# Performance work log

Measured on AMD Instinct MI355X. Metric: run time of the kernel, lower is better.

## Reference

```python
import jax, jax.numpy as jnp
import numpy as np

B, S, HID = 2, 2048, 2048
NUM_HEADS, NUM_KV = 32, 8
HEAD_DIM = HID // NUM_HEADS  # 64
GROUP = NUM_HEADS // NUM_KV  # 4
SCALE = 1.0 / np.sqrt(HEAD_DIM)


def rotate_half(x):
    x1, x2 = jnp.split(x, 2, axis=-1)
    return jnp.concatenate((-x2, x1), axis=-1)


def rope_tables(seq_len, dim):
    # NOTE: original repo buggily built the table over hidden_dim; the only
    # broadcast-consistent (and standard) interpretation is per-head dim.
    inv_freq = 1.0 / (10000.0 ** (jnp.arange(0, dim, 2, dtype=jnp.float32) / dim))
    t = jnp.arange(seq_len, dtype=jnp.float32)
    freqs = t[:, None] * inv_freq[None, :]          # (S, dim/2)
    emb = jnp.concatenate((freqs, freqs), axis=-1)  # (S, dim)
    return jnp.sin(emb), jnp.cos(emb)


def setup_inputs() -> dict:
    key = jax.random.key(0)
    ks = jax.random.split(key, 6)
    hidden_states = jax.random.normal(ks[0], (B, S, HID), dtype=jnp.float32)
    # causal additive mask (intent of the module's broken else-branch)
    causal = jnp.triu(jnp.full((S, S), -1e9, dtype=jnp.float32), k=1)
    attn_mask = causal[None, None]  # (1,1,S,S)
    init = lambda k, shp: jax.random.normal(k, shp, dtype=jnp.float32) * (1.0 / np.sqrt(shp[1]))
    wq = init(ks[1], (HID, HID))
    wk = init(ks[2], (NUM_KV * HEAD_DIM, HID))
    wv = init(ks[3], (NUM_KV * HEAD_DIM, HID))
    wo = init(ks[4], (HID, HID))
    return {"hidden_states": hidden_states, "attn_mask": attn_mask,
            "wq": wq, "wk": wk, "wv": wv, "wo": wo}


def reference(hidden_states, attn_mask, wq, wk, wv, wo):
    b, s, _ = hidden_states.shape
    q = (hidden_states @ wq.T).reshape(b, s, NUM_HEADS, HEAD_DIM)
    k = (hidden_states @ wk.T).reshape(b, s, NUM_KV, HEAD_DIM)
    v = (hidden_states @ wv.T).reshape(b, s, NUM_KV, HEAD_DIM)

    sin, cos = rope_tables(s, HEAD_DIM)        # (S, D)
    sin = sin[None, :, None, :]                # (1,S,1,D)
    cos = cos[None, :, None, :]
    q = q * cos + rotate_half(q) * sin
    k = k * cos + rotate_half(k) * sin

    # GQA without materializing repeat_interleave: split query heads as (kv, group)
    q = q.transpose(0, 2, 1, 3).reshape(b, NUM_KV, GROUP, s, HEAD_DIM)  # (B,K,G,S,D)
    k = k.transpose(0, 2, 1, 3)                                          # (B,K,S,D)
    v = v.transpose(0, 2, 1, 3)                                          # (B,K,S,D)

    scores = jnp.einsum('bkgqd,bksd->bkgqs', q, k) * SCALE  # (B,K,G,Sq,Sk)
    scores = scores + attn_mask[:, :, None]                 # broadcast (1,1,1,S,S)
    attn = jax.nn.softmax(scores, axis=-1)
    out = jnp.einsum('bkgqs,bksd->bkgqd', attn, v)          # (B,K,G,S,D)
    out = out.reshape(b, NUM_HEADS, s, HEAD_DIM).transpose(0, 2, 1, 3).reshape(b, s, HID)
    return out @ wo.T
```

## Files before the change

kernel.cpp:

```cpp
#include <hip/hip_runtime.h>
#include <hip/hip_bf16.h>

#define HIDDEN 2048
#define SEQ    2048
#define BATCH  2
#define NH     32
#define NKV    8
#define GRP    4
#define HD     64
#define KVDIM  512
#define NQKV   3072
#define SC2    0.18033688011112042f
#define NBANDS 32

typedef __attribute__((ext_vector_type(8))) short short8;
typedef __attribute__((ext_vector_type(4))) short short4v;
typedef __attribute__((ext_vector_type(4))) float f32x4;
typedef __attribute__((ext_vector_type(2))) float f32x2;
typedef __attribute__((ext_vector_type(4))) unsigned short us4;
typedef __attribute__((ext_vector_type(4))) float f4;

__device__ inline float bf2f(unsigned short u) {
    union { unsigned int i; float f; } x; x.i = ((unsigned int)u) << 16; return x.f;
}
__device__ inline unsigned short f2bf(float f) {
    union { float f; unsigned int i; } x; x.f = f;
    unsigned int r = x.i + 0x7fffu + ((x.i >> 16) & 1u);
    return (unsigned short)(r >> 16);
}

__device__ __forceinline__ f32x4 mfma16(short4v a, short4v b, f32x4 c) {
#if __has_builtin(__builtin_amdgcn_mfma_f32_16x16x16bf16_1k)
    return __builtin_amdgcn_mfma_f32_16x16x16bf16_1k(a, b, c, 0, 0, 0);
#elif __has_builtin(__builtin_amdgcn_mfma_f32_16x16x16_bf16)
    return __builtin_amdgcn_mfma_f32_16x16x16_bf16(a, b, c, 0, 0, 0);
#else
    asm volatile("v_mfma_f32_16x16x16_bf16 %0, %1, %2, %0" : "+v"(c) : "v"(a), "v"(b));
    return c;
#endif
}

__device__ __forceinline__ short4v pack4bf(float a, float b, float c, float d) {
    __hip_bfloat162 lo = __float22bfloat162_rn(make_float2(a, b));
    __hip_bfloat162 hi = __float22bfloat162_rn(make_float2(c, d));
    union { __hip_bfloat162 h2[2]; short4v s; } u;
    u.h2[0] = lo; u.h2[1] = hi;
    return u.s;
}

__global__ void detect_kernel(const unsigned short* __restrict__ hs, int* __restrict__ flag)
{
    int t = threadIdx.x;
    unsigned int e = hs[2 * t] & 0x7F80u;
    bool sane = (e >= 0x3800u) && (e <= 0x4100u);
    unsigned long long m = __ballot(sane);
    if (t == 0) *flag = (__popcll(m) >= 32) ? 0 : 1;
}

__global__ __launch_bounds__(256) void cvt_all(const void* __restrict__ a, const void* __restrict__ b,
                                               const void* __restrict__ c, const void* __restrict__ d,
                                               const void* __restrict__ e,
                                               unsigned short* __restrict__ dst,
                                               const int* __restrict__ flag)
{
    const int c0 = 2097152;
    const int c1 = c0 + 1048576;
    const int c2 = c1 + 262144;
    const int c3 = c2 + 262144;
    const int c4 = c3 + 1048576;
    int i = blockIdx.x * 256 + threadIdx.x;
    if (i >= c4) return;
    const void* src; int off;
    if (i < c0)      { src = a; off = i; }
    else if (i < c1) { src = b; off = i - c0; }
    else if (i < c2) { src = c; off = i - c1; }
    else if (i < c3) { src = d; off = i - c2; }
    else             { src = e; off = i - c3; }
    if (*flag) {
        f4 v = ((const f4*)src)[off];
        us4 o = { f2bf(v[0]), f2bf(v[1]), f2bf(v[2]), f2bf(v[3]) };
        ((us4*)dst)[i] = o;
    } else {
        ((us4*)dst)[i] = ((const us4*)src)[off];
    }
}

__global__ void rope_tbl_kernel(float* __restrict__ tbl)
{
    int i = blockIdx.x * blockDim.x + threadIdx.x;
    int s = i >> 5, d = i & 31;
    float f = (float)s * __expf(-(float)d * 0.28782313662425572f);
    float sn, c;
    sincosf(f, &sn, &c);
    tbl[i * 2]     = c;
    tbl[i * 2 + 1] = sn;
}

__global__ __launch_bounds__(256) void gemm128(const unsigned short* __restrict__ X,
                                               const unsigned short* __restrict__ W,
                                               void* __restrict__ Y0,
                                               unsigned short* __restrict__ Yk,
                                               unsigned short* __restrict__ Yv,
                                               const float* __restrict__ tbl,
                                               int N, int K,
                                               const int* __restrict__ flag, int mode)
{
    __shared__ unsigned short As[2][128 * 32];
    __shared__ unsigned short Bs[2][128 * 32];

    int tid  = threadIdx.x;
    int wave = tid >> 6;
    int lane = tid & 63;
    int l15  = lane & 15;
    int quad = lane >> 4;
    int wr   = wave >> 1;
    int wc   = wave & 1;
    int m0 = blockIdx.y * 128;
    int n0 = blockIdx.x * 128;

    const unsigned short* ga = X + (size_t)(m0 + (tid >> 2)) * K + (tid & 3) * 8;
    const unsigned short* gb = W + (size_t)(n0 + (tid >> 2)) * K + (tid & 3) * 8;
    const size_t rowskip = (size_t)64 * K;

#define GLDS(gp, lp) __builtin_amdgcn_global_load_lds( \
    (__attribute__((address_space(1))) void*)(gp), \
    (__attribute__((address_space(3))) void*)(lp), 16, 0, 0)

#define STAGEG(bi, k0v) do { \
    GLDS(ga + (k0v),           &As[bi][wave * 512]); \
    GLDS(ga + rowskip + (k0v), &As[bi][2048 + wave * 512]); \
    GLDS(gb + (k0v),           &Bs[bi][wave * 512]); \
    GLDS(gb + rowskip + (k0v), &Bs[bi][2048 + wave * 512]); \
} while (0)

    f32x4 acc[4][4];
#pragma unroll
    for (int i = 0; i < 4; ++i)
#pragma unroll
        for (int j = 0; j < 4; ++j) acc[i][j] = (f32x4){0.f, 0.f, 0.f, 0.f};

    STAGEG(0, 0);
    int nk = K >> 5;
    for (int it = 0; it < nk; ++it) {
        int bi = it & 1;
        __syncthreads();
        if (it + 1 < nk) STAGEG(bi ^ 1, (it + 1) * 32);

        short8 af[4], bfr[4];
#pragma unroll
        for (int mt = 0; mt < 4; ++mt)
            af[mt] = *(const short8*)&As[bi][(wr * 64 + mt * 16 + l15) * 32 + quad * 8];
#pragma unroll
        for (int nt = 0; nt < 4; ++nt)
            bfr[nt] = *(const short8*)&Bs[bi][(wc * 64 + nt * 16 + l15) * 32 + quad * 8];
#pragma unroll
        for (int mt = 0; mt < 4; ++mt)
#pragma unroll
            for (int nt = 0; nt < 4; ++nt)
                acc[mt][nt] = __builtin_amdgcn_mfma_f32_16x16x32_bf16(af[mt], bfr[nt], acc[mt][nt], 0, 0, 0);
    }
#undef STAGEG
#undef GLDS

    if (mode == 0) {
        int out_f32 = *flag;
#pragma unroll
        for (int mt = 0; mt < 4; ++mt)
#pragma unroll
            for (int nt = 0; nt < 4; ++nt)
#pragma unroll
                for (int r = 0; r < 4; ++r) {
                    size_t idx = (size_t)(m0 + wr * 64 + mt * 16 + quad * 4 + r) * N
                               + n0 + wc * 64 + nt * 16 + l15;
                    if (out_f32) ((float*)Y0)[idx] = acc[mt][nt][r];
                    else         ((unsigned short*)Y0)[idx] = f2bf(acc[mt][nt][r]);
                }
        return;
    }

    int nbase = n0 + wc * 64;
    if (nbase < HIDDEN) {
#pragma unroll
        for (int mt = 0; mt < 4; ++mt)
#pragma unroll
            for (int nt = 0; nt < 4; ++nt)
#pragma unroll
                for (int r = 0; r < 4; ++r) acc[mt][nt][r] *= SC2;
    }
    if (nbase < HIDDEN + KVDIM) {
#pragma unroll
        for (int mt = 0; mt < 4; ++mt)
#pragma unroll
            for (int r = 0; r < 4; ++r) {
                int s = (m0 + wr * 64 + mt * 16 + quad * 4 + r) & (SEQ - 1);
                f32x2 t0 = *(const f32x2*)&tbl[(s * 32 + l15) * 2];
                f32x2 t1 = *(const f32x2*)&tbl[(s * 32 + 16 + l15) * 2];
#pragma unroll
                for (int nt = 0; nt < 2; ++nt) {
                    float c  = nt ? t1[0] : t0[0];
                    float sn = nt ? t1[1] : t0[1];
                    float x1 = acc[mt][nt][r], x2 = acc[mt][nt + 2][r];
                    acc[mt][nt][r]     = x1 * c - x2 * sn;
                    acc[mt][nt + 2][r] = x2 * c + x1 * sn;
                }
            }
    }
    if (nbase < HIDDEN) {
        unsigned short* dst = (unsigned short*)Y0;
#pragma unroll
        for (int mt = 0; mt < 4; ++mt)
#pragma unroll
            for (int nt = 0; nt < 4; ++nt)
#pragma unroll
                for (int r = 0; r < 4; ++r)
                    dst[(size_t)(m0 + wr * 64 + mt * 16 + quad * 4 + r) * HIDDEN
                        + nbase + nt * 16 + l15] = f2bf(acc[mt][nt][r]);
    } else if (nbase < HIDDEN + KVDIM) {
        int cbase = nbase - HIDDEN;
#pragma unroll
        for (int mt = 0; mt < 4; ++mt)
#pragma unroll
            for (int nt = 0; nt < 4; ++nt)
#pragma unroll
                for (int r = 0; r < 4; ++r)
                    Yk[(size_t)(m0 + wr * 64 + mt * 16 + quad * 4 + r) * KVDIM
                       + cbase + nt * 16 + l15] = f2bf(acc[mt][nt][r]);
    } else {
        int kvh = (nbase - HIDDEN - KVDIM) >> 6;
#pragma unroll
        for (int mt = 0; mt < 4; ++mt) {
            int m = m0 + wr * 64 + mt * 16 + quad * 4;
            int bb = m >> 11, s = m & (SEQ - 1);
#pragma unroll
            for (int nt = 0; nt < 4; ++nt) {
                us4 pk = { f2bf(acc[mt][nt][0]), f2bf(acc[mt][nt][1]),
                           f2bf(acc[mt][nt][2]), f2bf(acc[mt][nt][3]) };
                *(us4*)&Yv[((size_t)(bb * NKV + kvh) * HD + nt * 16 + l15) * SEQ + s] = pk;
            }
        }
    }
}

__global__ __launch_bounds__(256, 4) void flash_attn(const unsigned short* __restrict__ q,
                                                     const unsigned short* __restrict__ k,
                                                     const unsigned short* __restrict__ vt,
                                                     unsigned short* __restrict__ o)
{
    __shared__ unsigned short Kd[2][64 * 64];
    __shared__ unsigned short Vd[2][64 * 64];

    int tid  = threadIdx.x;
    int lane = tid & 63;
    int wave = tid >> 6;
    int l15  = lane & 15;
    int quad = lane >> 4;
    int h7   = l15 & 7;
    int p  = blockIdx.x;
    int hp = blockIdx.y;
    int b  = blockIdx.z;
    int kv = hp >> 1;

    int srow = wave * 8 + (lane >> 3);
    int scol = ((lane & 7) ^ (lane >> 3)) * 8;
    const unsigned short* kgl = k + (size_t)(b * SEQ + srow) * KVDIM + kv * HD + scol;
    const unsigned short* vgl = vt + ((size_t)(b * NKV + kv) * HD + srow) * SEQ + scol;

#define GLDS(gp, lp) __builtin_amdgcn_global_load_lds( \
    (__attribute__((address_space(1))) void*)(gp), \
    (__attribute__((address_space(3))) void*)(lp), 16, 0, 0)

#define STAGE(bufi, j0v) do { \
    GLDS(kgl + (size_t)(j0v) * KVDIM,        &Kd[bufi][wave * 512]); \
    GLDS(kgl + (size_t)((j0v) + 32) * KVDIM, &Kd[bufi][2048 + wave * 512]); \
    GLDS(vgl + (j0v),                        &Vd[bufi][wave * 512]); \
    GLDS(vgl + (size_t)32 * SEQ + (j0v),     &Vd[bufi][2048 + wave * 512]); \
} while (0)

    for (int ph = 0; ph < 2; ++ph) {
        int band = ph ? (NBANDS - 1 - p) : p;
        int i0 = band * 64;
        int r0 = i0 + wave * 16;

        const unsigned short* qbase = q + (size_t)(b * SEQ + r0 + l15) * HIDDEN + hp * (2 * HD) + quad * 8;
        short8 aq00 = *(const short8*)(qbase);
        short8 aq01 = *(const short8*)(qbase + 32);
        short8 aq10 = *(const short8*)(qbase + 64);
        short8 aq11 = *(const short8*)(qbase + 96);

        float la00 = 0.f, la01 = 0.f, la02 = 0.f, la03 = 0.f;
        float la10 = 0.f, la11 = 0.f, la12 = 0.f, la13 = 0.f;
        f32x4 oacc0[4], oacc1[4];
#pragma unroll
        for (int t = 0; t < 4; ++t) {
            oacc0[t] = (f32x4){0.f, 0.f, 0.f, 0.f};
            oacc1[t] = (f32x4){0.f, 0.f, 0.f, 0.f};
        }

        int ig = r0 + l15;
        int ntiles = band + 1;
        STAGE(0, 0);

        for (int jt = 0; jt < ntiles; ++jt) {
            int buf = jt & 1;
            __syncthreads();
            if (jt + 1 < ntiles) STAGE(buf ^ 1, (jt + 1) * 64);
            int j0 = jt * 64;
            bool diag = (jt == band);
            const unsigned short* Kb = &Kd[buf][0];
            const unsigned short* Vb = &Vd[buf][0];

#pragma unroll
            for (int hf = 0; hf < 2; ++hf) {
                f32x4 s0[2], s1[2];
#pragma unroll
                for (int tt = 0; tt < 2; ++tt) {
                    int row = (hf * 2 + tt) * 16 + l15;
                    short8 ka0 = *(const short8*)&Kb[row * 64 + ((quad ^ h7) * 8)];
                    short8 ka1 = *(const short8*)&Kb[row * 64 + (((4 + quad) ^ h7) * 8)];
                    f32x4 z = {0.f, 0.f, 0.f, 0.f};
                    z = __builtin_amdgcn_mfma_f32_16x16x32_bf16(ka0, aq00, z, 0, 0, 0);
                    z = __builtin_amdgcn_mfma_f32_16x16x32_bf16(ka1, aq01, z, 0, 0, 0);
                    s0[tt] = z;
                    f32x4 w = {0.f, 0.f, 0.f, 0.f};
                    w = __builtin_amdgcn_mfma_f32_16x16x32_bf16(ka0, aq10, w, 0, 0, 0);
                    w = __builtin_amdgcn_mfma_f32_16x16x32_bf16(ka1, aq11, w, 0, 0, 0);
                    s1[tt] = w;
                }
                short4v ap0[2], ap1[2];
#pragma unroll
                for (int tt = 0; tt < 2; ++tt) {
                    float p0[4], p1[4];
#pragma unroll
                    for (int r = 0; r < 4; ++r) {
                        float e0 = exp2f(s0[tt][r]);
                        float e1 = exp2f(s1[tt][r]);
                        if (diag) {
                            int j = j0 + (hf * 2 + tt) * 16 + quad * 4 + r;
                            bool ok = (j <= ig);
                            e0 = ok ? e0 : 0.f;
                            e1 = ok ? e1 : 0.f;
                        }
                        p0[r] = e0; p1[r] = e1;
                    }
                    la00 += p0[0]; la01 += p0[1]; la02 += p0[2]; la03 += p0[3];
                    la10 += p1[0]; la11 += p1[1]; la12 += p1[2]; la13 += p1[3];
                    ap0[tt] = pack4bf(p0[0], p0[1], p0[2], p0[3]);
                    ap1[tt] = pack4bf(p1[0], p1[1], p1[2], p1[3]);
                }
#pragma unroll
                for (int dt = 0; dt < 4; ++dt) {
                    int vrow = dt * 16 + l15;
                    f32x4 z0 = oacc0[dt], z1 = oacc1[dt];
#pragma unroll
                    for (int tt = 0; tt < 2; ++tt) {
                        int kb = hf * 2 + tt;
                        int vcb = (kb * 32 + quad * 8) ^ (h7 << 4);
                        short4v vv = *(const short4v*)&Vb[vrow * 64 + (vcb >> 1)];
                        z0 = mfma16(vv, ap0[tt], z0);
                        z1 = mfma16(vv, ap1[tt], z1);
                    }
                    oacc0[dt] = z0; oacc1[dt] = z1;
                }
            }
        }

        float lr0 = (la00 + la01) + (la02 + la03);
        lr0 += __shfl_xor(lr0, 16, 64);
        lr0 += __shfl_xor(lr0, 32, 64);
        float lr1 = (la10 + la11) + (la12 + la13);
        lr1 += __shfl_xor(lr1, 16, 64);
        lr1 += __shfl_xor(lr1, 32, 64);
        float inv0 = 1.0f / lr0;
        float inv1 = 1.0f / lr1;
        unsigned short* obase = o + (size_t)(b * SEQ + r0 + l15) * HIDDEN + hp * (2 * HD) + quad * 4;
#pragma unroll
        for (int dt = 0; dt < 4; ++dt) {
            us4 pk0 = { f2bf(oacc0[dt][0] * inv0), f2bf(oacc0[dt][1] * inv0),
                        f2bf(oacc0[dt][2] * inv0), f2bf(oacc0[dt][3] * inv0) };
            *(us4*)(obase + dt * 16) = pk0;
            us4 pk1 = { f2bf(oacc1[dt][0] * inv1), f2bf(oacc1[dt][1] * inv1),
                        f2bf(oacc1[dt][2] * inv1), f2bf(oacc1[dt][3] * inv1) };
            *(us4*)(obase + HD + dt * 16) = pk1;
        }

        __syncthreads();
    }
#undef STAGE
#undef GLDS
}

extern "C" void kernel_launch(void* const* d_in, const int* in_sizes, int n_in,
                              void* d_out, int out_size, void* d_ws, size_t ws_size,
                              hipStream_t stream)
{
    const void* hs = d_in[0];
    const void* wq = d_in[2];
    const void* wk = d_in[3];
    const void* wv = d_in[4];
    const void* wo = d_in[5];

    const int M = BATCH * SEQ;
    int* flag = (int*)d_ws;
    unsigned short* base = (unsigned short*)((char*)d_ws + 256);
    unsigned short* hsb  = base;
    unsigned short* wqkv = hsb + (size_t)M * HIDDEN;
    unsigned short* wob  = wqkv + (size_t)NQKV * HIDDEN;
    unsigned short* qbuf = wob + (size_t)HIDDEN * HIDDEN;
    unsigned short* kbuf = qbuf + (size_t)M * HIDDEN;
    unsigned short* vbuf = kbuf + (size_t)M * KVDIM;
    unsigned short* abuf = vbuf + (size_t)M * KVDIM;
    float* tbl = (float*)(abuf + (size_t)M * HIDDEN);

    dim3 blk(256);
    detect_kernel<<<1, 64, 0, stream>>>((const unsigned short*)hs, flag);
    rope_tbl_kernel<<<256, blk, 0, stream>>>(tbl);

    const int total4 = 2097152 + 1048576 + 262144 + 262144 + 1048576;
    cvt_all<<<(total4 + 255) / 256, blk, 0, stream>>>(hs, wq, wk, wv, wo, hsb, flag);

    gemm128<<<dim3(NQKV / 128, M / 128), blk, 0, stream>>>(hsb, wqkv, qbuf, kbuf, vbuf,
                                                           tbl, NQKV, HIDDEN, flag, 1);

    flash_attn<<<dim3(NBANDS / 2, NH / 2, BATCH), blk, 0, stream>>>(qbuf, kbuf, vbuf, abuf);

    gemm128<<<dim3(HIDDEN / 128, M / 128), blk, 0, stream>>>(abuf, wob, d_out, nullptr, nullptr,
                                                             tbl, HIDDEN, HIDDEN, flag, 0);
}
```

Before: 344.3 us.

## Triple-buffer GEMM LDS stages to keep two global loads in flight

Moves the bf16 GEMM's shared-memory staging from double to triple buffering and prefetches two k-tiles ahead. A partial `s_waitcnt vmcnt(4)` lets the next tile's async global-to-LDS loads stay outstanding while the current tile is computed. A scheduling barrier stops the compiler from reordering across the sync point. The aim is to hide more global-load latency behind MFMA work, at the cost of 50% more LDS per block, which could lower occupancy.

```diff
diff --git a/kernel.cpp b/kernel.cpp
--- a/kernel.cpp
+++ b/kernel.cpp
@@ -105,8 +105,8 @@
                                                int N, int K,
                                                const int* __restrict__ flag, int mode)
 {
-    __shared__ unsigned short As[2][128 * 32];
-    __shared__ unsigned short Bs[2][128 * 32];
+    __shared__ unsigned short As[3][128 * 32];
+    __shared__ unsigned short Bs[3][128 * 32];
 
     int tid  = threadIdx.x;
     int wave = tid >> 6;
@@ -133,32 +133,45 @@
     GLDS(gb + rowskip + (k0v), &Bs[bi][2048 + wave * 512]); \
 } while (0)
 
+#define GEMM_BODY(bi) do { \
+    short8 af[4], bfr[4]; \
+    _Pragma("unroll") \
+    for (int mt = 0; mt < 4; ++mt) \
+        af[mt] = *(const short8*)&As[bi][(wr * 64 + mt * 16 + l15) * 32 + quad * 8]; \
+    _Pragma("unroll") \
+    for (int nt = 0; nt < 4; ++nt) \
+        bfr[nt] = *(const short8*)&Bs[bi][(wc * 64 + nt * 16 + l15) * 32 + quad * 8]; \
+    _Pragma("unroll") \
+    for (int mt = 0; mt < 4; ++mt) \
+        _Pragma("unroll") \
+        for (int nt = 0; nt < 4; ++nt) \
+            acc[mt][nt] = __builtin_amdgcn_mfma_f32_16x16x32_bf16(af[mt], bfr[nt], acc[mt][nt], 0, 0, 0); \
+} while (0)
+
     f32x4 acc[4][4];
 #pragma unroll
     for (int i = 0; i < 4; ++i)
 #pragma unroll
         for (int j = 0; j < 4; ++j) acc[i][j] = (f32x4){0.f, 0.f, 0.f, 0.f};
 
+    int nk = K >> 5;
     STAGEG(0, 0);
-    int nk = K >> 5;
-    for (int it = 0; it < nk; ++it) {
-        int bi = it & 1;
-        __syncthreads();
-        if (it + 1 < nk) STAGEG(bi ^ 1, (it + 1) * 32);
-
-        short8 af[4], bfr[4];
-#pragma unroll
-        for (int mt = 0; mt < 4; ++mt)
-            af[mt] = *(const short8*)&As[bi][(wr * 64 + mt * 16 + l15) * 32 + quad * 8];
-#pragma unroll
-        for (int nt = 0; nt < 4; ++nt)
-            bfr[nt] = *(const short8*)&Bs[bi][(wc * 64 + nt * 16 + l15) * 32 + quad * 8];
-#pragma unroll
-        for (int mt = 0; mt < 4; ++mt)
-#pragma unroll
-            for (int nt = 0; nt < 4; ++nt)
-                acc[mt][nt] = __builtin_amdgcn_mfma_f32_16x16x32_bf16(af[mt], bfr[nt], acc[mt][nt], 0, 0, 0);
-    }
+    STAGEG(1, 32);
+    int cur = 0;
+    for (int it = 0; it < nk - 1; ++it) {
+        asm volatile("s_waitcnt vmcnt(4)" ::: "memory");
+        __builtin_amdgcn_s_barrier();
+        __builtin_amdgcn_sched_barrier(0);
+        int nb = cur + 2; if (nb >= 3) nb -= 3;
+        if (it + 2 < nk) STAGEG(nb, (it + 2) * 32);
+        GEMM_BODY(cur);
+        cur = (cur == 2) ? 0 : cur + 1;
+    }
+    asm volatile("s_waitcnt vmcnt(0)" ::: "memory");
+    __builtin_amdgcn_s_barrier();
+    __builtin_amdgcn_sched_barrier(0);
+    GEMM_BODY(cur);
+#undef GEMM_BODY
 #undef STAGEG
 #undef GLDS
 
```

Measured after the change: 347.0 us. Within noise of the previous version (+0.8%).
